# Kernel tuning notes

Hardware: AMD Instinct MI355X
Metric: run time of the kernel (lower is better)

The kernel has to match this reference:

```python
import jax, jax.numpy as jnp
import numpy as np
from jax import lax

B, D, K = 65536, 256, 32  # batch, num_latent_dims, flow_depth


def setup_inputs() -> dict:
    key = jax.random.key(0)
    k1, k2, k3, k4, k5 = jax.random.split(key, 5)
    X = jax.random.normal(k1, (B, D), dtype=jnp.float32)
    h = jax.random.normal(k2, (B, D), dtype=jnp.float32)  # passed through, unused by planar math
    u = jax.random.normal(k3, (K, D), dtype=jnp.float32) * 0.1
    w = jax.random.normal(k4, (K, D), dtype=jnp.float32) * 0.1
    b = jax.random.normal(k5, (K,), dtype=jnp.float32) * 0.1
    return {"X": X, "h": h, "u": u, "w": w, "b": b}


def _planar_chain(z0, u, w, b):
    """Sequential planar normalizing flow: z_{k+1} = z_k + u_hat_k * tanh(w_k.z_k + b_k)."""

    def step(z, params):
        u_k, w_k, b_k = params  # (D,), (D,), scalar
        # enforce invertibility: u_hat so that w.u_hat >= -1
        wu = jnp.dot(w_k, u_k)
        u_hat = u_k + (jax.nn.softplus(wu) - 1.0 - wu) * w_k / jnp.dot(w_k, w_k)
        lin = z @ w_k + b_k              # (B,)
        t = jnp.tanh(lin)                # (B,)
        z_new = z + t[:, None] * u_hat[None, :]
        # psi = (1 - t^2) w ; log|det J| = log|1 + psi.u_hat|
        log_det = jnp.log(jnp.abs(1.0 + (1.0 - t * t) * jnp.dot(w_k, u_hat)) + 1e-8)
        return z_new, log_det

    z_final, log_dets = lax.scan(step, z0, (u, w, b))
    return z_final, log_dets  # (B, D), (K, B)


def reference(X, h, u, w, b):
    z = X.reshape(X.shape[0], X.shape[1])  # view(B, D, -1) then view(B, D) -> (B, D)
    z_final, log_det_jacobians = _planar_chain(z, u, w, b)
    return z_final, log_det_jacobians
```

## Files before the change

### kernel.cpp

```cpp
#include <hip/hip_runtime.h>


typedef __attribute__((ext_vector_type(8))) short short8;
typedef __attribute__((ext_vector_type(4))) float f32x4;

#define B_ 65536
#define D_ 256
#define ROWS 128
#define GRID (B_ / ROWS)

#define WSB_WH 0
#define WSB_WL 16896
#define WSB_UTH 33792
#define WSB_UTL 54272
#define WSB_G 74752
#define WSB_C 78848

#define OFF_P 8448
#define OFF_G 17696
#define OFF_C 18752
#define OFF_B 18784
#define LDSF 18816
#define WH_H 0
#define WL_H 8448
#define UH_H 0
#define UL_H 10240
#define XH_H 25152
#define XL_H 30272

__device__ __forceinline__ void bfsplit(float x, unsigned short& h, unsigned short& l) {
  unsigned xb = __float_as_uint(x) & 0xffff0000u;
  h = (unsigned short)(xb >> 16);
  float r = x - __uint_as_float(xb);
  l = (unsigned short)(__float_as_uint(r) >> 16);
}

__global__ __launch_bounds__(256) void nf_gen(const float* __restrict__ u_in,
                                              const float* __restrict__ w_in,
                                              float* __restrict__ ws) {
  __shared__ float wTg[8192];
  __shared__ float ug[8192];
  __shared__ float wu_s[32], ww_s[32], coefs_s[32];
  const int t = threadIdx.x;
  {
    const int k = t & 31, d0 = (t >> 5) * 32;
    const float4* wp = (const float4*)(w_in + k * 256 + d0);
#pragma unroll
    for (int q = 0; q < 8; ++q) {
      float4 v = wp[q];
      wTg[(d0 + q * 4 + 0) * 32 + k] = v.x;
      wTg[(d0 + q * 4 + 1) * 32 + k] = v.y;
      wTg[(d0 + q * 4 + 2) * 32 + k] = v.z;
      wTg[(d0 + q * 4 + 3) * 32 + k] = v.w;
    }
#pragma unroll
    for (int q = 0; q < 8; ++q)
      ((float4*)ug)[t + 256 * q] = ((const float4*)u_in)[t + 256 * q];
  }
  __syncthreads();
  const int k = t & 31, jg = t >> 5;
  float m1[4] = {0.f, 0.f, 0.f, 0.f}, m2[4] = {0.f, 0.f, 0.f, 0.f};
#pragma unroll 4
  for (int dc = 0; dc < 64; ++dc) {
    float wk[4];
    float4 wj[4], uj[4];
#pragma unroll
    for (int i = 0; i < 4; ++i) wk[i] = wTg[(dc * 4 + i) * 32 + k];
#pragma unroll
    for (int i = 0; i < 4; ++i) wj[i] = *(const float4*)&wTg[(dc * 4 + i) * 32 + jg * 4];
#pragma unroll
    for (int i = 0; i < 4; ++i) uj[i] = *(const float4*)&ug[(jg * 4 + i) * 256 + dc * 4];
#pragma unroll
    for (int i = 0; i < 4; ++i) {
      m1[i] = fmaf(uj[i].x, wk[0], m1[i]);
      m1[i] = fmaf(uj[i].y, wk[1], m1[i]);
      m1[i] = fmaf(uj[i].z, wk[2], m1[i]);
      m1[i] = fmaf(uj[i].w, wk[3], m1[i]);
    }
    const float* w0 = (const float*)&wj[0];
    const float* w1 = (const float*)&wj[1];
    const float* w2 = (const float*)&wj[2];
    const float* w3 = (const float*)&wj[3];
#pragma unroll
    for (int i = 0; i < 4; ++i) {
      m2[i] = fmaf(w0[i], wk[0], m2[i]);
      m2[i] = fmaf(w1[i], wk[1], m2[i]);
      m2[i] = fmaf(w2[i], wk[2], m2[i]);
      m2[i] = fmaf(w3[i], wk[3], m2[i]);
    }
  }
  if ((k >> 2) == jg) {
    wu_s[k] = m1[k & 3];
    ww_s[k] = m2[k & 3];
  }
  __syncthreads();
  if (t < 32) {
    float wu = wu_s[t], ww = ww_s[t];
    float sp = fmaxf(wu, 0.f) + log1pf(__expf(-fabsf(wu)));
    coefs_s[t] = (sp - 1.f - wu) / ww;
    ((float*)((char*)ws + WSB_C))[t] = sp - 1.f;
  }
  __syncthreads();
  {
    float* gws = (float*)((char*)ws + WSB_G);
#pragma unroll
    for (int i = 0; i < 4; ++i)
      gws[k * 32 + jg * 4 + i] = fmaf(coefs_s[jg * 4 + i], m2[i], m1[i]);
  }
  {
    const int k2 = t >> 3, d0 = (t & 7) * 32;
    const float ck = coefs_s[k2];
    unsigned short* whp = (unsigned short*)((char*)ws + WSB_WH);
    unsigned short* wlp = (unsigned short*)((char*)ws + WSB_WL);
    unsigned short* uthp = (unsigned short*)((char*)ws + WSB_UTH);
    unsigned short* utlp = (unsigned short*)((char*)ws + WSB_UTL);
    const float4* wp2 = (const float4*)(w_in + k2 * 256 + d0);
    const float4* up2 = (const float4*)(u_in + k2 * 256 + d0);
#pragma unroll
    for (int q = 0; q < 8; ++q) {
      float4 wv = wp2[q], uv = up2[q];
      const float wf[4] = {wv.x, wv.y, wv.z, wv.w};
      const float uf[4] = {uv.x, uv.y, uv.z, uv.w};
#pragma unroll
      for (int i = 0; i < 4; ++i) {
        unsigned short hh, ll;
        bfsplit(wf[i], hh, ll);
        whp[k2 * 264 + d0 + q * 4 + i] = hh;
        wlp[k2 * 264 + d0 + q * 4 + i] = ll;
        float uhv = fmaf(ck, wf[i], uf[i]);
        bfsplit(uhv, hh, ll);
        uthp[(d0 + q * 4 + i) * 40 + k2] = hh;
        utlp[(d0 + q * 4 + i) * 40 + k2] = ll;
      }
    }
  }
}

__global__ __launch_bounds__(256) void nf_fused(const float* __restrict__ X,
                                                const float* __restrict__ b_in,
                                                const float* __restrict__ ws,
                                                float* __restrict__ out) {
  __shared__ __align__(16) float lds[LDSF];
  unsigned short* ldsH = (unsigned short*)lds;

  const int t = threadIdx.x;
  const int lane = t & 63;
  const int wv = t >> 6;
  const int ln15 = lane & 15;
  const int g = lane >> 4;
  const int g8 = g * 8, g4 = g * 4;
  const int row0 = blockIdx.x * ROWS;

  {
    const uint4* wsrc = (const uint4*)((const char*)ws + WSB_WH);
    uint4* wdst = (uint4*)lds;
#pragma unroll
    for (int i = 0; i < 8; ++i) wdst[t + 256 * i] = wsrc[t + 256 * i];
    if (t < 64) wdst[2048 + t] = wsrc[2048 + t];
  }
#pragma unroll
  for (int i = 0; i < 4; ++i) {
    const int e = t * 4 + i;
    lds[OFF_G + (e >> 5) * 33 + (e & 31)] = ((const float*)((const char*)ws + WSB_G))[e];
  }
  if (t < 32) {
    lds[OFF_C + t] = ((const float*)((const char*)ws + WSB_C))[t];
    lds[OFF_B + t] = b_in[t];
  }

  const int srow = t >> 1;
  const int sdh = (t & 1) * 16;
  float4 xr[4];
  auto load_stage = [&](int cc) {
    const float4* src = (const float4*)(X + (size_t)(row0 + srow) * 256 + cc * 32 + sdh);
#pragma unroll
    for (int j = 0; j < 4; ++j) xr[j] = src[j];
  };
  auto store_stage = [&]() {
    float xf[16];
#pragma unroll
    for (int j = 0; j < 4; ++j) {
      xf[j * 4 + 0] = xr[j].x; xf[j * 4 + 1] = xr[j].y;
      xf[j * 4 + 2] = xr[j].z; xf[j * 4 + 3] = xr[j].w;
    }
    short8 h0, h1, l0, l1;
#pragma unroll
    for (int e = 0; e < 8; ++e) {
      unsigned short hh, ll;
      bfsplit(xf[e], hh, ll);
      h0[e] = (short)hh; l0[e] = (short)ll;
      bfsplit(xf[8 + e], hh, ll);
      h1[e] = (short)hh; l1[e] = (short)ll;
    }
    *(short8*)&ldsH[XH_H + srow * 40 + sdh] = h0;
    *(short8*)&ldsH[XH_H + srow * 40 + sdh + 8] = h1;
    *(short8*)&ldsH[XL_H + srow * 40 + sdh] = l0;
    *(short8*)&ldsH[XL_H + srow * 40 + sdh + 8] = l1;
  };

  f32x4 acc[2][2];
#pragma unroll
  for (int m = 0; m < 2; ++m)
#pragma unroll
    for (int n = 0; n < 2; ++n) acc[m][n] = (f32x4){0.f, 0.f, 0.f, 0.f};

  load_stage(0);
  for (int cc = 0; cc < 8; ++cc) {
    store_stage();
    __syncthreads();
    if (cc < 7) load_stage(cc + 1);
    short8 ah[2], al[2], bh[2], bl[2];
#pragma unroll
    for (int m = 0; m < 2; ++m) {
      const int hidx = XH_H + ((wv * 2 + m) * 16 + ln15) * 40 + g8;
      ah[m] = *(const short8*)&ldsH[hidx];
      al[m] = *(const short8*)&ldsH[hidx + (XL_H - XH_H)];
    }
#pragma unroll
    for (int n = 0; n < 2; ++n) {
      const int widx = (n * 16 + ln15) * 264 + cc * 32 + g8;
      bh[n] = *(const short8*)&ldsH[WH_H + widx];
      bl[n] = *(const short8*)&ldsH[WL_H + widx];
    }
#pragma unroll
    for (int m = 0; m < 2; ++m)
#pragma unroll
      for (int n = 0; n < 2; ++n) {
        acc[m][n] = __builtin_amdgcn_mfma_f32_16x16x32_bf16(ah[m], bh[n], acc[m][n], 0, 0, 0);
        acc[m][n] = __builtin_amdgcn_mfma_f32_16x16x32_bf16(ah[m], bl[n], acc[m][n], 0, 0, 0);
        acc[m][n] = __builtin_amdgcn_mfma_f32_16x16x32_bf16(al[m], bh[n], acc[m][n], 0, 0, 0);
      }
    __syncthreads();
  }

#pragma unroll
  for (int m = 0; m < 2; ++m)
#pragma unroll
    for (int n = 0; n < 2; ++n)
#pragma unroll
      for (int q = 0; q < 4; ++q)
        lds[OFF_P + (n * 16 + ln15) * 129 + ((wv * 2 + m) * 16 + g4 + q)] = acc[m][n][q];
  __syncthreads();

  if (t < 128) {
    float pfull[32];
#pragma unroll
    for (int j = 0; j < 32; ++j) pfull[j] = lds[OFF_P + j * 129 + t] + lds[OFF_B + j];
    float tvv[32];
#pragma unroll
    for (int kk = 0; kk < 32; ++kk) {
      float la = pfull[kk], lb2 = 0.f;
      const float* gp = &lds[OFF_G + kk * 33];
#pragma unroll
      for (int j = 0; j + 1 < kk; j += 2) {
        la = fmaf(tvv[j], gp[j], la);
        lb2 = fmaf(tvv[j + 1], gp[j + 1], lb2);
      }
      if (kk & 1) la = fmaf(tvv[kk - 1], gp[kk - 1], la);
      float lin = la + lb2;
      float e = __expf(2.f * lin);
      float tk = 1.f - 2.f / (e + 1.f);
      tvv[kk] = tk;
      float val = fabsf(fmaf(1.f - tk * tk, lds[OFF_C + kk], 1.f)) + 1e-8f;
      out[(size_t)B_ * D_ + (size_t)kk * B_ + row0 + t] = __logf(val);
    }
#pragma unroll
    for (int q = 0; q < 4; ++q) {
      short8 th, tl;
#pragma unroll
      for (int i = 0; i < 8; ++i) {
        unsigned short hh, ll;
        bfsplit(tvv[q * 8 + i], hh, ll);
        th[i] = (short)hh;
        tl[i] = (short)ll;
      }
      *(short8*)&ldsH[XH_H + t * 40 + q * 8] = th;
      *(short8*)&ldsH[XL_H + t * 40 + q * 8] = tl;
    }
  }
  __syncthreads();

  {
    const uint4* usrc = (const uint4*)((const char*)ws + WSB_UTH);
    uint4* udst = (uint4*)lds;
#pragma unroll
    for (int i = 0; i < 10; ++i) udst[t + 256 * i] = usrc[t + 256 * i];
  }
  __syncthreads();

  short8 tah[2], tal[2];
#pragma unroll
  for (int m = 0; m < 2; ++m) {
    const int hidx = XH_H + ((wv * 2 + m) * 16 + ln15) * 40 + g8;
    tah[m] = *(const short8*)&ldsH[hidx];
    tal[m] = *(const short8*)&ldsH[hidx + (XL_H - XH_H)];
  }
  for (int Nt = 0; Nt < 16; ++Nt) {
    const int uidx = (Nt * 16 + ln15) * 40 + g8;
    short8 bh = *(const short8*)&ldsH[UH_H + uidx];
    short8 bl = *(const short8*)&ldsH[UL_H + uidx];
    const int col = Nt * 16 + ln15;
#pragma unroll
    for (int m = 0; m < 2; ++m) {
      const size_t rbase = (size_t)row0 + (wv * 2 + m) * 16 + g4;
      f32x4 c;
#pragma unroll
      for (int q = 0; q < 4; ++q) c[q] = X[(rbase + q) * 256 + col];
      c = __builtin_amdgcn_mfma_f32_16x16x32_bf16(tah[m], bh, c, 0, 0, 0);
      c = __builtin_amdgcn_mfma_f32_16x16x32_bf16(tah[m], bl, c, 0, 0, 0);
      c = __builtin_amdgcn_mfma_f32_16x16x32_bf16(tal[m], bh, c, 0, 0, 0);
#pragma unroll
      for (int q = 0; q < 4; ++q) out[(rbase + q) * 256 + col] = c[q];
    }
  }
}

extern "C" void kernel_launch(void* const* d_in, const int* in_sizes, int n_in,
                              void* d_out, int out_size, void* d_ws, size_t ws_size,
                              hipStream_t stream) {
  const float* X = (const float*)d_in[0];
  const float* u = (const float*)d_in[2];
  const float* w = (const float*)d_in[3];
  const float* b = (const float*)d_in[4];
  float* out = (float*)d_out;
  float* ws = (float*)d_ws;

  nf_gen<<<1, 256, 0, stream>>>(u, w, ws);
  nf_fused<<<GRID, 256, 0, stream>>>(X, b, ws, out);
}
```

Measured before the change: 211.3 us.

## Halve rows per block, double threads, read recurrence constants from global

Each block now covers 64 rows with 512 threads, and each wave owns one 16x16 MFMA tile instead of a 2x2 set, which cuts per-thread registers and LDS use so more blocks can be resident. The G matrix, C coefficients and bias are read straight from global memory (cache) in the serial tanh recurrence instead of being staged in LDS. The tanh bf16 split is written per element inside the loop. In exchange, the weight tiles are staged into LDS twice as often across the grid, and only 64 of 512 threads run the serial recurrence, so that phase could dominate.

```diff
diff --git a/kernel.cpp b/kernel.cpp
--- a/kernel.cpp
+++ b/kernel.cpp
@@ -6,7 +6,8 @@
 
 #define B_ 65536
 #define D_ 256
-#define ROWS 128
+#define ROWS 64
+#define NTHR 512
 #define GRID (B_ / ROWS)
 
 #define WSB_WH 0
@@ -16,17 +17,14 @@
 #define WSB_G 74752
 #define WSB_C 78848
 
-#define OFF_P 8448
-#define OFF_G 17696
-#define OFF_C 18752
-#define OFF_B 18784
-#define LDSF 18816
 #define WH_H 0
 #define WL_H 8448
 #define UH_H 0
 #define UL_H 10240
-#define XH_H 25152
-#define XL_H 30272
+#define XH_H 20480
+#define XL_H 23040
+#define LDS_HALVES 25600
+#define P_STR 65
 
 __device__ __forceinline__ void bfsplit(float x, unsigned short& h, unsigned short& l) {
   unsigned xb = __float_as_uint(x) & 0xffff0000u;
@@ -136,12 +134,12 @@
   }
 }
 
-__global__ __launch_bounds__(256) void nf_fused(const float* __restrict__ X,
-                                                const float* __restrict__ b_in,
-                                                const float* __restrict__ ws,
-                                                float* __restrict__ out) {
-  __shared__ __align__(16) float lds[LDSF];
-  unsigned short* ldsH = (unsigned short*)lds;
+__global__ __launch_bounds__(NTHR, 6) void nf_fused(const float* __restrict__ X,
+                                                    const float* __restrict__ b_in,
+                                                    const float* __restrict__ ws,
+                                                    float* __restrict__ out) {
+  __shared__ __align__(16) unsigned short ldsH[LDS_HALVES];
+  float* ldsF = (float*)ldsH;
 
   const int t = threadIdx.x;
   const int lane = t & 63;
@@ -149,108 +147,72 @@
   const int ln15 = lane & 15;
   const int g = lane >> 4;
   const int g8 = g * 8, g4 = g * 4;
+  const int slab = wv >> 1;
+  const int nt0 = wv & 1;
   const int row0 = blockIdx.x * ROWS;
 
   {
     const uint4* wsrc = (const uint4*)((const char*)ws + WSB_WH);
-    uint4* wdst = (uint4*)lds;
-#pragma unroll
-    for (int i = 0; i < 8; ++i) wdst[t + 256 * i] = wsrc[t + 256 * i];
+    uint4* wdst = (uint4*)ldsH;
+#pragma unroll
+    for (int i = 0; i < 4; ++i) wdst[t + 512 * i] = wsrc[t + 512 * i];
     if (t < 64) wdst[2048 + t] = wsrc[2048 + t];
   }
-#pragma unroll
-  for (int i = 0; i < 4; ++i) {
-    const int e = t * 4 + i;
-    lds[OFF_G + (e >> 5) * 33 + (e & 31)] = ((const float*)((const char*)ws + WSB_G))[e];
-  }
-  if (t < 32) {
-    lds[OFF_C + t] = ((const float*)((const char*)ws + WSB_C))[t];
-    lds[OFF_B + t] = b_in[t];
-  }
-
-  const int srow = t >> 1;
-  const int sdh = (t & 1) * 16;
-  float4 xr[4];
+
+  const int srow = t >> 3;
+  const int sd = (t & 7) * 4;
+  float4 xr;
   auto load_stage = [&](int cc) {
-    const float4* src = (const float4*)(X + (size_t)(row0 + srow) * 256 + cc * 32 + sdh);
-#pragma unroll
-    for (int j = 0; j < 4; ++j) xr[j] = src[j];
+    xr = *(const float4*)(X + (size_t)(row0 + srow) * 256 + cc * 32 + sd);
   };
   auto store_stage = [&]() {
-    float xf[16];
-#pragma unroll
-    for (int j = 0; j < 4; ++j) {
-      xf[j * 4 + 0] = xr[j].x; xf[j * 4 + 1] = xr[j].y;
-      xf[j * 4 + 2] = xr[j].z; xf[j * 4 + 3] = xr[j].w;
-    }
-    short8 h0, h1, l0, l1;
-#pragma unroll
-    for (int e = 0; e < 8; ++e) {
-      unsigned short hh, ll;
-      bfsplit(xf[e], hh, ll);
-      h0[e] = (short)hh; l0[e] = (short)ll;
-      bfsplit(xf[8 + e], hh, ll);
-      h1[e] = (short)hh; l1[e] = (short)ll;
-    }
-    *(short8*)&ldsH[XH_H + srow * 40 + sdh] = h0;
-    *(short8*)&ldsH[XH_H + srow * 40 + sdh + 8] = h1;
-    *(short8*)&ldsH[XL_H + srow * 40 + sdh] = l0;
-    *(short8*)&ldsH[XL_H + srow * 40 + sdh + 8] = l1;
+    const float xf[4] = {xr.x, xr.y, xr.z, xr.w};
+    unsigned short h[4], l[4];
+#pragma unroll
+    for (int e = 0; e < 4; ++e) bfsplit(xf[e], h[e], l[e]);
+    *(uint2*)&ldsH[XH_H + srow * 40 + sd] =
+        make_uint2((unsigned)h[0] | ((unsigned)h[1] << 16),
+                   (unsigned)h[2] | ((unsigned)h[3] << 16));
+    *(uint2*)&ldsH[XL_H + srow * 40 + sd] =
+        make_uint2((unsigned)l[0] | ((unsigned)l[1] << 16),
+                   (unsigned)l[2] | ((unsigned)l[3] << 16));
   };
 
-  f32x4 acc[2][2];
-#pragma unroll
-  for (int m = 0; m < 2; ++m)
-#pragma unroll
-    for (int n = 0; n < 2; ++n) acc[m][n] = (f32x4){0.f, 0.f, 0.f, 0.f};
-
+  f32x4 acc = (f32x4){0.f, 0.f, 0.f, 0.f};
   load_stage(0);
   for (int cc = 0; cc < 8; ++cc) {
     store_stage();
     __syncthreads();
     if (cc < 7) load_stage(cc + 1);
-    short8 ah[2], al[2], bh[2], bl[2];
-#pragma unroll
-    for (int m = 0; m < 2; ++m) {
-      const int hidx = XH_H + ((wv * 2 + m) * 16 + ln15) * 40 + g8;
-      ah[m] = *(const short8*)&ldsH[hidx];
-      al[m] = *(const short8*)&ldsH[hidx + (XL_H - XH_H)];
-    }
-#pragma unroll
-    for (int n = 0; n < 2; ++n) {
-      const int widx = (n * 16 + ln15) * 264 + cc * 32 + g8;
-      bh[n] = *(const short8*)&ldsH[WH_H + widx];
-      bl[n] = *(const short8*)&ldsH[WL_H + widx];
-    }
-#pragma unroll
-    for (int m = 0; m < 2; ++m)
-#pragma unroll
-      for (int n = 0; n < 2; ++n) {
-        acc[m][n] = __builtin_amdgcn_mfma_f32_16x16x32_bf16(ah[m], bh[n], acc[m][n], 0, 0, 0);
-        acc[m][n] = __builtin_amdgcn_mfma_f32_16x16x32_bf16(ah[m], bl[n], acc[m][n], 0, 0, 0);
-        acc[m][n] = __builtin_amdgcn_mfma_f32_16x16x32_bf16(al[m], bh[n], acc[m][n], 0, 0, 0);
-      }
+    const int hidx = XH_H + (slab * 16 + ln15) * 40 + g8;
+    short8 ah = *(const short8*)&ldsH[hidx];
+    short8 al = *(const short8*)&ldsH[hidx + (XL_H - XH_H)];
+    const int widx = (nt0 * 16 + ln15) * 264 + cc * 32 + g8;
+    short8 bh = *(const short8*)&ldsH[WH_H + widx];
+    short8 bl = *(const short8*)&ldsH[WL_H + widx];
+    acc = __builtin_amdgcn_mfma_f32_16x16x32_bf16(ah, bh, acc, 0, 0, 0);
+    acc = __builtin_amdgcn_mfma_f32_16x16x32_bf16(ah, bl, acc, 0, 0, 0);
+    acc = __builtin_amdgcn_mfma_f32_16x16x32_bf16(al, bh, acc, 0, 0, 0);
     __syncthreads();
   }
 
-#pragma unroll
-  for (int m = 0; m < 2; ++m)
-#pragma unroll
-    for (int n = 0; n < 2; ++n)
-#pragma unroll
-      for (int q = 0; q < 4; ++q)
-        lds[OFF_P + (n * 16 + ln15) * 129 + ((wv * 2 + m) * 16 + g4 + q)] = acc[m][n][q];
-  __syncthreads();
-
-  if (t < 128) {
-    float pfull[32];
-#pragma unroll
-    for (int j = 0; j < 32; ++j) pfull[j] = lds[OFF_P + j * 129 + t] + lds[OFF_B + j];
+  {
+    const int kcol = nt0 * 16 + ln15;
+#pragma unroll
+    for (int q = 0; q < 4; ++q)
+      ldsF[kcol * P_STR + slab * 16 + g4 + q] = acc[q];
+  }
+  __syncthreads();
+
+  if (t < 64) {
+    const float* gws = (const float*)((const char*)ws + WSB_G);
+    const float* cws = (const float*)((const char*)ws + WSB_C);
     float tvv[32];
 #pragma unroll
     for (int kk = 0; kk < 32; ++kk) {
-      float la = pfull[kk], lb2 = 0.f;
-      const float* gp = &lds[OFF_G + kk * 33];
+      float la = ldsF[kk * P_STR + t] + b_in[kk];
+      float lb2 = 0.f;
+      const float* gp = gws + kk * 32;
 #pragma unroll
       for (int j = 0; j + 1 < kk; j += 2) {
         la = fmaf(tvv[j], gp[j], la);
@@ -261,54 +223,42 @@
       float e = __expf(2.f * lin);
       float tk = 1.f - 2.f / (e + 1.f);
       tvv[kk] = tk;
-      float val = fabsf(fmaf(1.f - tk * tk, lds[OFF_C + kk], 1.f)) + 1e-8f;
+      unsigned short hh, ll;
+      bfsplit(tk, hh, ll);
+      ldsH[XH_H + t * 40 + kk] = hh;
+      ldsH[XL_H + t * 40 + kk] = ll;
+      float val = fabsf(fmaf(1.f - tk * tk, cws[kk], 1.f)) + 1e-8f;
       out[(size_t)B_ * D_ + (size_t)kk * B_ + row0 + t] = __logf(val);
     }
-#pragma unroll
-    for (int q = 0; q < 4; ++q) {
-      short8 th, tl;
-#pragma unroll
-      for (int i = 0; i < 8; ++i) {
-        unsigned short hh, ll;
-        bfsplit(tvv[q * 8 + i], hh, ll);
-        th[i] = (short)hh;
-        tl[i] = (short)ll;
-      }
-      *(short8*)&ldsH[XH_H + t * 40 + q * 8] = th;
-      *(short8*)&ldsH[XL_H + t * 40 + q * 8] = tl;
-    }
   }
   __syncthreads();
 
   {
     const uint4* usrc = (const uint4*)((const char*)ws + WSB_UTH);
-    uint4* udst = (uint4*)lds;
-#pragma unroll
-    for (int i = 0; i < 10; ++i) udst[t + 256 * i] = usrc[t + 256 * i];
-  }
-  __syncthreads();
-
-  short8 tah[2], tal[2];
-#pragma unroll
-  for (int m = 0; m < 2; ++m) {
-    const int hidx = XH_H + ((wv * 2 + m) * 16 + ln15) * 40 + g8;
-    tah[m] = *(const short8*)&ldsH[hidx];
-    tal[m] = *(const short8*)&ldsH[hidx + (XL_H - XH_H)];
-  }
-  for (int Nt = 0; Nt < 16; ++Nt) {
-    const int uidx = (Nt * 16 + ln15) * 40 + g8;
-    short8 bh = *(const short8*)&ldsH[UH_H + uidx];
-    short8 bl = *(const short8*)&ldsH[UL_H + uidx];
-    const int col = Nt * 16 + ln15;
-#pragma unroll
-    for (int m = 0; m < 2; ++m) {
-      const size_t rbase = (size_t)row0 + (wv * 2 + m) * 16 + g4;
+    uint4* udst = (uint4*)ldsH;
+#pragma unroll
+    for (int i = 0; i < 5; ++i) udst[t + 512 * i] = usrc[t + 512 * i];
+  }
+  __syncthreads();
+
+  {
+    const int hidx = XH_H + (slab * 16 + ln15) * 40 + g8;
+    short8 tah = *(const short8*)&ldsH[hidx];
+    short8 tal = *(const short8*)&ldsH[hidx + (XL_H - XH_H)];
+    const size_t rbase = (size_t)row0 + slab * 16 + g4;
+#pragma unroll 2
+    for (int i = 0; i < 8; ++i) {
+      const int nt = nt0 + 2 * i;
+      const int uidx = (nt * 16 + ln15) * 40 + g8;
+      short8 bh = *(const short8*)&ldsH[UH_H + uidx];
+      short8 bl = *(const short8*)&ldsH[UL_H + uidx];
+      const int col = nt * 16 + ln15;
       f32x4 c;
 #pragma unroll
       for (int q = 0; q < 4; ++q) c[q] = X[(rbase + q) * 256 + col];
-      c = __builtin_amdgcn_mfma_f32_16x16x32_bf16(tah[m], bh, c, 0, 0, 0);
-      c = __builtin_amdgcn_mfma_f32_16x16x32_bf16(tah[m], bl, c, 0, 0, 0);
-      c = __builtin_amdgcn_mfma_f32_16x16x32_bf16(tal[m], bh, c, 0, 0, 0);
+      c = __builtin_amdgcn_mfma_f32_16x16x32_bf16(tah, bh, c, 0, 0, 0);
+      c = __builtin_amdgcn_mfma_f32_16x16x32_bf16(tah, bl, c, 0, 0, 0);
+      c = __builtin_amdgcn_mfma_f32_16x16x32_bf16(tal, bh, c, 0, 0, 0);
 #pragma unroll
       for (int q = 0; q < 4; ++q) out[(rbase + q) * 256 + col] = c[q];
     }
@@ -326,5 +276,5 @@
   float* ws = (float*)d_ws;
 
   nf_gen<<<1, 256, 0, stream>>>(u, w, ws);
-  nf_fused<<<GRID, 256, 0, stream>>>(X, b, ws, out);
-}
+  nf_fused<<<GRID, NTHR, 0, stream>>>(X, b, ws, out);
+}
```

Result: slower. 220.3 us (+4.3%).
